# Performance work log

Hardware: AMD Instinct MI355X
Metric: run time of the kernel (lower is better)

The kernel has to match this reference:

```python
import jax, jax.numpy as jnp
import numpy as np


def setup_inputs() -> dict:
    key = jax.random.key(0)
    k1, k2 = jax.random.split(key, 2)
    B, S, H, E = 4, 4096, 4096, 64
    h = jax.random.normal(k1, (B, S, H), dtype=jnp.float32)
    # gate weight as in nn.Linear(hidden_dim, num_experts): W [E, H], bias [E]
    W = jax.random.normal(k2, (E, H), dtype=jnp.float32) * (1.0 / np.sqrt(H))
    b = jnp.zeros((E,), dtype=jnp.float32)
    return {"h": h, "W": W, "b": b, "k": 2}


def reference(h, W, b, k):
    # eval-mode forward (self.training == False, so no gaussian noise)
    # logits: [B, S, E]
    logits = jnp.einsum('bsh,eh->bse', h, W) + b
    E = logits.shape[-1]
    B, S = h.shape[0], h.shape[1]

    # top-k over experts, softmax over the k selected logits
    topk_vals, topk_idx = jax.lax.top_k(logits, k)          # [B, S, k]
    topk_scores = jax.nn.softmax(topk_vals, axis=-1)        # [B, S, k]

    # scatter softmaxed scores back into a zero [B, S, E] tensor
    # (topk indices are distinct, so sum-of-one-hots == scatter)
    route_weights = jnp.sum(
        jax.nn.one_hot(topk_idx, E, dtype=topk_scores.dtype) * topk_scores[..., None],
        axis=-2,
    )  # [B, S, E]

    # aux-loss statistics
    importance = jax.nn.softmax(logits, axis=-1).sum(axis=(0, 1))            # [E]
    load = (route_weights > 0).astype(jnp.float32).sum(axis=(0, 1)) / (B * S)  # [E]
    aux_loss = jnp.mean(importance * load * (E ** 2))
    return route_weights, aux_loss
```

## Files before the change

kernel.cpp:

```cpp
#include <hip/hip_runtime.h>
#include <hip/hip_bf16.h>
#include <math.h>

typedef __attribute__((ext_vector_type(8))) short  short8;
typedef __attribute__((ext_vector_type(4))) float  float4v;

#define NE 64
#define FLAG_CAP 8192
#define EPS_TIE 2e-4f
#define KSPLIT 4

#define BARRIER  asm volatile("s_barrier" ::: "memory")
#define WAITV(n) asm volatile("s_waitcnt vmcnt(" #n ")" ::: "memory")

__device__ __forceinline__ unsigned short f2bf(float x){
  unsigned u = __float_as_uint(x);
  return (unsigned short)((u + 0x7fffu + ((u>>16)&1u)) >> 16);
}
__device__ __forceinline__ float bf2f(unsigned short h){
  return __uint_as_float(((unsigned)h)<<16);
}
__device__ __forceinline__ float warp_sum64(float v){
  #pragma unroll
  for (int off=1; off<64; off<<=1) v += __shfl_xor(v, off, 64);
  return v;
}

__device__ __forceinline__ void gld16(void* lds, const void* g){
  __builtin_amdgcn_global_load_lds(
      (const __attribute__((address_space(1))) unsigned int*)g,
      (__attribute__((address_space(3))) unsigned int*)lds,
      16, 0, 0);
}

__global__ __launch_bounds__(256) void prep_w(
    const float* __restrict__ W, unsigned short* __restrict__ whi,
    unsigned short* __restrict__ wlo, float* __restrict__ zbuf, int K)
{
  if (blockIdx.x == 0){
    #pragma unroll
    for (int i=0;i<5;++i){
      const int idx = threadIdx.x + i*256;
      if (idx < 1025) zbuf[idx] = 0.f;
    }
  }
  const int id = blockIdx.x*256 + threadIdx.x;
  const int nfrag = (K/32)*4*64;
  if (id >= nfrag) return;
  const int lane = id & 63, te = (id>>6)&3, ks = id>>8;
  const int e  = te*16 + (lane&15);
  const int k0 = ks*32 + ((lane>>4)<<3);
  const float* src = W + (size_t)e*K + k0;
  short8 h8, l8;
  #pragma unroll
  for (int j=0;j<8;++j){
    float x = src[j];
    unsigned short hb = f2bf(x);
    h8[j] = (short)hb;
    l8[j] = (short)f2bf(x - bf2f(hb));
  }
  const size_t off = (size_t)id*8;
  *(short8*)(whi + off) = h8;
  *(short8*)(wlo + off) = l8;
}

__device__ __forceinline__ void cvt8b(const float4& c, const float4& d,
                                      short8& hi, short8& lo){
  const float f[8] = {c.x,c.y,c.z,c.w,d.x,d.y,d.z,d.w};
  union { short8 s; unsigned u[4]; } H, L;
  #pragma unroll
  for (int p=0;p<4;++p){
    float2 v = make_float2(f[2*p], f[2*p+1]);
    __hip_bfloat162 hb = __float22bfloat162_rn(v);
    H.u[p] = *reinterpret_cast<unsigned*>(&hb);
    float2 back = __bfloat1622float2(hb);
    float2 res = make_float2(v.x - back.x, v.y - back.y);
    __hip_bfloat162 lb = __float22bfloat162_rn(res);
    L.u[p] = *reinterpret_cast<unsigned*>(&lb);
  }
  hi = H.s; lo = L.s;
}

#define MFMA3(AH, AL, BH, BL, ACC)                                          \
  ACC = __builtin_amdgcn_mfma_f32_16x16x32_bf16(AH, BH, ACC, 0,0,0);        \
  ACC = __builtin_amdgcn_mfma_f32_16x16x32_bf16(AH, BL, ACC, 0,0,0);        \
  ACC = __builtin_amdgcn_mfma_f32_16x16x32_bf16(AL, BH, ACC, 0,0,0);

__global__ __launch_bounds__(256) void gemm_cnt(
    const float* __restrict__ hp, const unsigned short* __restrict__ whi,
    const unsigned short* __restrict__ wlo, float* __restrict__ part,
    int K, long M, int tiles)
{
  __shared__ float          As[2][64*32];
  __shared__ unsigned short Bs[2][8*512];

  const int tid = threadIdx.x;
  const int l = tid & 63, w = tid >> 6;
  const int tok0  = blockIdx.x * 64;
  const int slice = blockIdx.y;
  const int kbase = slice * (tiles*32);
  const int r16 = l & 15, kg = l >> 4;

  float4v acc[4];
  #pragma unroll
  for (int te=0;te<4;++te) acc[te] = (float4v){0.f,0.f,0.f,0.f};

  const unsigned short* bsel[2] = { whi, wlo };
  const int srcblkA = (l&7) ^ (l>>3);

  auto STAGE = [&](int buf, int t){
    #pragma unroll
    for (int i=0;i<2;++i){
      const int row = w*16 + i*8 + (l>>3);
      const float* src = hp + (size_t)(tok0 + row)*K + kbase + t*32 + (srcblkA<<2);
      gld16((void*)(As[buf] + w*512 + i*256), (const void*)src);
    }
    #pragma unroll
    for (int i=0;i<2;++i){
      const int u = w*2 + i;
      const int te = u >> 1, d = u & 1;
      const unsigned short* src = bsel[d]
          + ((size_t)(slice*tiles + t))*2048 + te*512 + (size_t)l*8;
      gld16((void*)(Bs[buf] + u*512), (const void*)src);
    }
  };

  auto COMPUTE = [&](int buf){
    const float* arow = As[buf] + (w*16 + r16)*32;
    const int c0 = kg*2, sw = r16 & 7;
    float4 a0 = *(const float4*)(arow + (((c0  ) ^ sw) << 2));
    float4 a1 = *(const float4*)(arow + (((c0+1) ^ sw) << 2));
    short8 Ah, Al;
    cvt8b(a0, a1, Ah, Al);
    #pragma unroll
    for (int te=0;te<4;++te){
      short8 Bh = *(const short8*)(Bs[buf] + (te*2+0)*512 + l*8);
      short8 Bl = *(const short8*)(Bs[buf] + (te*2+1)*512 + l*8);
      MFMA3(Ah, Al, Bh, Bl, acc[te]);
    }
  };

  STAGE(0, 0);
  STAGE(1, 1);
  WAITV(4); BARRIER;
  int t = 0;
  for (; t < tiles-2; ++t){
    COMPUTE(t&1);
    BARRIER;
    STAGE(t&1, t+2);
    WAITV(4); BARRIER;
  }
  COMPUTE(t&1);
  WAITV(0); BARRIER;
  COMPUTE((t+1)&1);

  float* dst = part + (size_t)slice*M*NE;
  #pragma unroll
  for (int te=0;te<4;++te)
    #pragma unroll
    for (int r=0;r<4;++r){
      const int tok = tok0 + w*16 + (kg<<2) + r;
      dst[(size_t)tok*NE + te*16 + r16] = acc[te][r];
    }
}

__global__ __launch_bounds__(256) void router_finish2(
    const float* __restrict__ part, const float* __restrict__ bp,
    float* __restrict__ outp, float* __restrict__ imp8,
    float* __restrict__ cnt8, int* __restrict__ flagCnt,
    int* __restrict__ flagList, long M)
{
  __shared__ float red[2][4][64];
  const int tid = threadIdx.x;
  const int w = tid >> 6, lane = tid & 63;
  const long base = (long)blockIdx.x*16 + w*4;
  const float bias = bp[lane];
  float impL = 0.f, cntL = 0.f;

  #pragma unroll 1
  for (int it=0; it<4; ++it){
    const long t = base + it;
    float v = part[t*NE + lane];
    v += part[(size_t)M*NE   + t*NE + lane];
    v += part[(size_t)M*NE*2 + t*NE + lane];
    v += part[(size_t)M*NE*3 + t*NE + lane];
    v += bias;
    float m1 = v; int i1 = lane;
    #pragma unroll
    for (int off=1; off<64; off<<=1){
      float ov = __shfl_xor(m1, off, 64);
      int   oi = __shfl_xor(i1, off, 64);
      if (ov > m1 || (ov == m1 && oi < i1)){ m1 = ov; i1 = oi; }
    }
    float vm = (lane == i1) ? -3.4e38f : v;
    float m2 = vm; int i2 = lane;
    #pragma unroll
    for (int off=1; off<64; off<<=1){
      float ov = __shfl_xor(m2, off, 64);
      int   oi = __shfl_xor(i2, off, 64);
      if (ov > m2 || (ov == m2 && oi < i2)){ m2 = ov; i2 = oi; }
    }
    float vm3 = (lane==i1 || lane==i2) ? -3.4e38f : v;
    float m3 = vm3;
    #pragma unroll
    for (int off=1; off<64; off<<=1) m3 = fmaxf(m3, __shfl_xor(m3, off, 64));
    if ((m2 - m3) < EPS_TIE && lane == 0){
      int idx = atomicAdd(flagCnt, 1);
      if (idx < FLAG_CAP) flagList[idx] = (int)t;
    }
    const float ex = __expf(m2 - m1);
    const float s1 = 1.f / (1.f + ex);
    const float s2 = ex * s1;
    const float p = __expf(v - m1);
    const float S = warp_sum64(p);
    impL += p / S;
    const float rw = (lane==i1) ? s1 : ((lane==i2) ? s2 : 0.f);
    outp[t*NE + lane] = rw;
    if (lane==i1 || lane==i2) cntL += 1.f;
  }
  red[0][w][lane] = impL;
  red[1][w][lane] = cntL;
  __syncthreads();
  if (tid < 64){
    float s = red[0][0][tid] + red[0][1][tid] + red[0][2][tid] + red[0][3][tid];
    float c = red[1][0][tid] + red[1][1][tid] + red[1][2][tid] + red[1][3][tid];
    const int g = (blockIdx.x & 7) << 6;
    atomicAdd(&imp8[g + tid], s);
    atomicAdd(&cnt8[g + tid], c);
  }
}

__global__ __launch_bounds__(256) void fixup_aux(
    const float* __restrict__ hp, const float* __restrict__ Wp,
    const float* __restrict__ bp, float* __restrict__ outp,
    const int* __restrict__ flagCnt, const int* __restrict__ flagList,
    const float* __restrict__ imp8, const float* __restrict__ cnt8,
    float* __restrict__ auxp, float scale, int K)
{
  __shared__ float hrow[4096];
  __shared__ float lg[NE];
  if (blockIdx.x == 0 && threadIdx.x < 64){
    float s = 0.f, c = 0.f;
    #pragma unroll
    for (int g=0; g<8; ++g){
      s += imp8[(g<<6) + threadIdx.x];
      c += cnt8[(g<<6) + threadIdx.x];
    }
    float v = s * c;
    v = warp_sum64(v);
    if (threadIdx.x == 0) auxp[0] = v * scale;
  }
  int n = *flagCnt; if (n > FLAG_CAP) n = FLAG_CAP;
  const int e   = threadIdx.x >> 2;
  const int sub = threadIdx.x & 3;
  const int lane = threadIdx.x & 63;

  for (int f = blockIdx.x; f < n; f += gridDim.x){
    const int tok = flagList[f];
    const float* hr = hp + (size_t)tok*K;
    #pragma unroll
    for (int c=0; c<4; ++c){
      const int idx = threadIdx.x*4 + c*1024;
      *(float4*)&hrow[idx] = *(const float4*)(hr + idx);
    }
    __syncthreads();
    const float* wr = Wp + (size_t)e*K;
    float s = 0.f;
    for (int it=0; it<64; ++it){
      const int k0 = it*64 + sub*16;
      #pragma unroll
      for (int u=0; u<4; ++u){
        float4 wv = *(const float4*)(wr + k0 + u*4);
        float4 hv = *(const float4*)(&hrow[k0 + u*4]);
        s = fmaf(hv.x, wv.x, s); s = fmaf(hv.y, wv.y, s);
        s = fmaf(hv.z, wv.z, s); s = fmaf(hv.w, wv.w, s);
      }
    }
    s += __shfl_xor(s, 1, 64);
    s += __shfl_xor(s, 2, 64);
    if (sub == 0) lg[e] = s + bp[e];
    __syncthreads();
    if (threadIdx.x < 64){
      const float v = lg[lane];
      float m1 = v; int i1 = lane;
      #pragma unroll
      for (int off=1; off<64; off<<=1){
        float ov = __shfl_xor(m1, off, 64);
        int   oi = __shfl_xor(i1, off, 64);
        if (ov > m1 || (ov == m1 && oi < i1)){ m1 = ov; i1 = oi; }
      }
      float vm = (lane == i1) ? -3.4e38f : v;
      float m2 = vm; int i2 = lane;
      #pragma unroll
      for (int off=1; off<64; off<<=1){
        float ov = __shfl_xor(m2, off, 64);
        int   oi = __shfl_xor(i2, off, 64);
        if (ov > m2 || (ov == m2 && oi < i2)){ m2 = ov; i2 = oi; }
      }
      const float ex = __expf(m2 - m1);
      const float s1 = 1.f / (1.f + ex);
      const float s2 = ex * s1;
      const float rw = (lane==i1) ? s1 : ((lane==i2) ? s2 : 0.f);
      outp[(size_t)tok * NE + lane] = rw;
    }
    __syncthreads();
  }
}

extern "C" void kernel_launch(void* const* d_in, const int* in_sizes, int n_in,
                              void* d_out, int out_size, void* d_ws, size_t ws_size,
                              hipStream_t stream){
  const float* hp = (const float*)d_in[0];
  const float* Wp = (const float*)d_in[1];
  const float* bp = (const float*)d_in[2];
  const int  E = in_sizes[2];
  const int  K = in_sizes[1] / E;
  const long M = (long)in_sizes[0] / K;

  float* outp = (float*)d_out;
  float* auxp = outp + (size_t)M * E;

  char* ws = (char*)d_ws;
  float* imp8     = (float*)(ws + 0);
  float* cnt8     = (float*)(ws + 2048);
  int*   flagCnt  = (int*)  (ws + 4096);
  int*   flagList = (int*)  (ws + 4160);
  unsigned short* whi = (unsigned short*)(ws + 65536);
  unsigned short* wlo = (unsigned short*)(ws + 65536 + 524288);
  float* part     = (float*)(ws + 1114112);

  const int nfragBlocks = ((K/32)*4*64 + 255)/256;
  const int tiles = (K / KSPLIT) / 32;

  prep_w<<<dim3(nfragBlocks), dim3(256), 0, stream>>>(Wp, whi, wlo, (float*)ws, K);
  gemm_cnt<<<dim3((int)(M/64), KSPLIT), dim3(256), 0, stream>>>(hp, whi, wlo, part, K, M, tiles);
  router_finish2<<<dim3((int)(M/16)), dim3(256), 0, stream>>>(part, bp, outp, imp8, cnt8,
                                                              flagCnt, flagList, M);
  fixup_aux<<<dim3(128), dim3(256), 0, stream>>>(hp, Wp, bp, outp, flagCnt, flagList,
                                                 imp8, cnt8, auxp, (float)E/(float)M, K);
}
```

Before: 91.75 us.

## Double gate GEMM token tile to 128 and split waves over tokens and experts

Each block of the split-K gating GEMM now covers 128 tokens instead of 64. Each wave computes a 64-token by 32-expert sub-tile with 4x2 accumulators instead of 16 tokens by all 64 experts. This reuses the B (weight) fragments across four A row-tiles per wave and halves B staging per token. The trade-off is that the grid shrinks by half, LDS use per block grows, and register pressure rises, which may reduce latency hiding on the memory-bound load of h.

Result: slower. 94.61 us (+3.1%).

```diff
diff --git a/kernel.cpp b/kernel.cpp
--- a/kernel.cpp
+++ b/kernel.cpp
@@ -9,6 +9,7 @@
 #define FLAG_CAP 8192
 #define EPS_TIE 2e-4f
 #define KSPLIT 4
+#define TOKB 128
 
 #define BARRIER  asm volatile("s_barrier" ::: "memory")
 #define WAITV(n) asm volatile("s_waitcnt vmcnt(" #n ")" ::: "memory")
@@ -91,29 +92,33 @@
     const unsigned short* __restrict__ wlo, float* __restrict__ part,
     int K, long M, int tiles)
 {
-  __shared__ float          As[2][64*32];
+  __shared__ float          As[2][TOKB*32];
   __shared__ unsigned short Bs[2][8*512];
 
   const int tid = threadIdx.x;
   const int l = tid & 63, w = tid >> 6;
-  const int tok0  = blockIdx.x * 64;
+  const int tok0  = blockIdx.x * TOKB;
   const int slice = blockIdx.y;
   const int kbase = slice * (tiles*32);
   const int r16 = l & 15, kg = l >> 4;
-
-  float4v acc[4];
-  #pragma unroll
-  for (int te=0;te<4;++te) acc[te] = (float4v){0.f,0.f,0.f,0.f};
+  const int th = w >> 1;
+  const int eh = w & 1;
+
+  float4v acc[4][2];
+  #pragma unroll
+  for (int m=0;m<4;++m)
+    #pragma unroll
+    for (int lt=0;lt<2;++lt) acc[m][lt] = (float4v){0.f,0.f,0.f,0.f};
 
   const unsigned short* bsel[2] = { whi, wlo };
   const int srcblkA = (l&7) ^ (l>>3);
 
   auto STAGE = [&](int buf, int t){
     #pragma unroll
-    for (int i=0;i<2;++i){
-      const int row = w*16 + i*8 + (l>>3);
+    for (int i=0;i<4;++i){
+      const int row = w*32 + i*8 + (l>>3);
       const float* src = hp + (size_t)(tok0 + row)*K + kbase + t*32 + (srcblkA<<2);
-      gld16((void*)(As[buf] + w*512 + i*256), (const void*)src);
+      gld16((void*)(As[buf] + w*1024 + i*256), (const void*)src);
     }
     #pragma unroll
     for (int i=0;i<2;++i){
@@ -126,29 +131,37 @@
   };
 
   auto COMPUTE = [&](int buf){
-    const float* arow = As[buf] + (w*16 + r16)*32;
+    short8 Bh[2], Bl[2];
+    #pragma unroll
+    for (int lt=0; lt<2; ++lt){
+      const int te = eh*2 + lt;
+      Bh[lt] = *(const short8*)(Bs[buf] + (te*2+0)*512 + l*8);
+      Bl[lt] = *(const short8*)(Bs[buf] + (te*2+1)*512 + l*8);
+    }
     const int c0 = kg*2, sw = r16 & 7;
-    float4 a0 = *(const float4*)(arow + (((c0  ) ^ sw) << 2));
-    float4 a1 = *(const float4*)(arow + (((c0+1) ^ sw) << 2));
-    short8 Ah, Al;
-    cvt8b(a0, a1, Ah, Al);
-    #pragma unroll
-    for (int te=0;te<4;++te){
-      short8 Bh = *(const short8*)(Bs[buf] + (te*2+0)*512 + l*8);
-      short8 Bl = *(const short8*)(Bs[buf] + (te*2+1)*512 + l*8);
-      MFMA3(Ah, Al, Bh, Bl, acc[te]);
+    #pragma unroll
+    for (int m=0;m<4;++m){
+      const float* arow = As[buf] + (th*64 + m*16 + r16)*32;
+      float4 a0 = *(const float4*)(arow + (((c0  ) ^ sw) << 2));
+      float4 a1 = *(const float4*)(arow + (((c0+1) ^ sw) << 2));
+      short8 Ah, Al;
+      cvt8b(a0, a1, Ah, Al);
+      #pragma unroll
+      for (int lt=0; lt<2; ++lt){
+        MFMA3(Ah, Al, Bh[lt], Bl[lt], acc[m][lt]);
+      }
     }
   };
 
   STAGE(0, 0);
   STAGE(1, 1);
-  WAITV(4); BARRIER;
+  WAITV(6); BARRIER;
   int t = 0;
   for (; t < tiles-2; ++t){
     COMPUTE(t&1);
     BARRIER;
     STAGE(t&1, t+2);
-    WAITV(4); BARRIER;
+    WAITV(6); BARRIER;
   }
   COMPUTE(t&1);
   WAITV(0); BARRIER;
@@ -156,12 +169,14 @@
 
   float* dst = part + (size_t)slice*M*NE;
   #pragma unroll
-  for (int te=0;te<4;++te)
-    #pragma unroll
-    for (int r=0;r<4;++r){
-      const int tok = tok0 + w*16 + (kg<<2) + r;
-      dst[(size_t)tok*NE + te*16 + r16] = acc[te][r];
-    }
+  for (int m=0;m<4;++m)
+    #pragma unroll
+    for (int lt=0;lt<2;++lt)
+      #pragma unroll
+      for (int r=0;r<4;++r){
+        const int tok = tok0 + th*64 + m*16 + (kg<<2) + r;
+        dst[(size_t)tok*NE + (eh*2+lt)*16 + r16] = acc[m][lt][r];
+      }
 }
 
 __global__ __launch_bounds__(256) void router_finish2(
@@ -333,7 +348,7 @@
   const int tiles = (K / KSPLIT) / 32;
 
   prep_w<<<dim3(nfragBlocks), dim3(256), 0, stream>>>(Wp, whi, wlo, (float*)ws, K);
-  gemm_cnt<<<dim3((int)(M/64), KSPLIT), dim3(256), 0, stream>>>(hp, whi, wlo, part, K, M, tiles);
+  gemm_cnt<<<dim3((int)(M/TOKB), KSPLIT), dim3(256), 0, stream>>>(hp, whi, wlo, part, K, M, tiles);
   router_finish2<<<dim3((int)(M/16)), dim3(256), 0, stream>>>(part, bp, outp, imp8, cnt8,
                                                               flagCnt, flagList, M);
   fixup_aux<<<dim3(128), dim3(256), 0, stream>>>(hp, Wp, bp, outp, flagCnt, flagList,
```

## Fuse router epilogue into GEMM and drop split-K partial buffer

Applied to the files above, without the earlier changes.

Removes the split-K decomposition so each block computes full-K logits for 64 tokens with 8 waves splitting tokens and experts. Logits go to shared memory and the top-2/softmax/importance epilogue runs in the same kernel, eliminating the partial-sum buffer round trip and one launch. A third staging buffer deepens prefetch. The trade-off is fewer blocks (one per token tile) and less parallelism for streaming h, which may lower achieved bandwidth.

Result: slower. 130.1 us (+41.8%).

```diff
diff --git a/kernel.cpp b/kernel.cpp
--- a/kernel.cpp
+++ b/kernel.cpp
@@ -8,7 +8,7 @@
 #define NE 64
 #define FLAG_CAP 8192
 #define EPS_TIE 2e-4f
-#define KSPLIT 4
+#define TOKB 64
 
 #define BARRIER  asm volatile("s_barrier" ::: "memory")
 #define WAITV(n) asm volatile("s_waitcnt vmcnt(" #n ")" ::: "memory")
@@ -86,127 +86,112 @@
   ACC = __builtin_amdgcn_mfma_f32_16x16x32_bf16(AH, BL, ACC, 0,0,0);        \
   ACC = __builtin_amdgcn_mfma_f32_16x16x32_bf16(AL, BH, ACC, 0,0,0);
 
-__global__ __launch_bounds__(256) void gemm_cnt(
+__global__ __launch_bounds__(512) void gemm_router(
     const float* __restrict__ hp, const unsigned short* __restrict__ whi,
-    const unsigned short* __restrict__ wlo, float* __restrict__ part,
-    int K, long M, int tiles)
+    const unsigned short* __restrict__ wlo, const float* __restrict__ bp,
+    float* __restrict__ outp, float* __restrict__ imp8, float* __restrict__ cnt8,
+    int* __restrict__ flagCnt, int* __restrict__ flagList, int K, long M, int tiles)
 {
-  __shared__ float          As[2][64*32];
-  __shared__ unsigned short Bs[2][8*512];
+  __shared__ float          As[3][TOKB*32];
+  __shared__ unsigned short Bs[3][8*512];
+  __shared__ float          lg[TOKB][NE];
+  __shared__ float          red[2][8][64];
 
   const int tid = threadIdx.x;
   const int l = tid & 63, w = tid >> 6;
-  const int tok0  = blockIdx.x * 64;
-  const int slice = blockIdx.y;
-  const int kbase = slice * (tiles*32);
+  const int tok0 = blockIdx.x * TOKB;
   const int r16 = l & 15, kg = l >> 4;
-
-  float4v acc[4];
-  #pragma unroll
-  for (int te=0;te<4;++te) acc[te] = (float4v){0.f,0.f,0.f,0.f};
+  const int th = w >> 1;
+  const int eh = w & 1;
+
+  float4v acc[2];
+  acc[0] = (float4v){0.f,0.f,0.f,0.f};
+  acc[1] = (float4v){0.f,0.f,0.f,0.f};
 
   const unsigned short* bsel[2] = { whi, wlo };
   const int srcblkA = (l&7) ^ (l>>3);
 
   auto STAGE = [&](int buf, int t){
-    #pragma unroll
-    for (int i=0;i<2;++i){
-      const int row = w*16 + i*8 + (l>>3);
-      const float* src = hp + (size_t)(tok0 + row)*K + kbase + t*32 + (srcblkA<<2);
-      gld16((void*)(As[buf] + w*512 + i*256), (const void*)src);
-    }
-    #pragma unroll
-    for (int i=0;i<2;++i){
-      const int u = w*2 + i;
-      const int te = u >> 1, d = u & 1;
-      const unsigned short* src = bsel[d]
-          + ((size_t)(slice*tiles + t))*2048 + te*512 + (size_t)l*8;
-      gld16((void*)(Bs[buf] + u*512), (const void*)src);
-    }
+    const int row = w*8 + (l>>3);
+    const float* srcA = hp + (size_t)(tok0 + row)*K + t*32 + (srcblkA<<2);
+    gld16((void*)(As[buf] + w*256), (const void*)srcA);
+    const unsigned short* srcB = bsel[w & 1]
+        + (size_t)t*2048 + (w>>1)*512 + (size_t)l*8;
+    gld16((void*)(Bs[buf] + w*512), (const void*)srcB);
   };
 
   auto COMPUTE = [&](int buf){
-    const float* arow = As[buf] + (w*16 + r16)*32;
+    short8 Bh[2], Bl[2];
+    #pragma unroll
+    for (int lt=0; lt<2; ++lt){
+      const int te = eh*2 + lt;
+      Bh[lt] = *(const short8*)(Bs[buf] + (te*2+0)*512 + l*8);
+      Bl[lt] = *(const short8*)(Bs[buf] + (te*2+1)*512 + l*8);
+    }
+    const float* arow = As[buf] + (th*16 + r16)*32;
     const int c0 = kg*2, sw = r16 & 7;
     float4 a0 = *(const float4*)(arow + (((c0  ) ^ sw) << 2));
     float4 a1 = *(const float4*)(arow + (((c0+1) ^ sw) << 2));
     short8 Ah, Al;
     cvt8b(a0, a1, Ah, Al);
     #pragma unroll
-    for (int te=0;te<4;++te){
-      short8 Bh = *(const short8*)(Bs[buf] + (te*2+0)*512 + l*8);
-      short8 Bl = *(const short8*)(Bs[buf] + (te*2+1)*512 + l*8);
-      MFMA3(Ah, Al, Bh, Bl, acc[te]);
+    for (int lt=0; lt<2; ++lt){
+      MFMA3(Ah, Al, Bh[lt], Bl[lt], acc[lt]);
     }
   };
 
-  STAGE(0, 0);
-  STAGE(1, 1);
+  STAGE(0,0); STAGE(1,1); STAGE(2,2);
   WAITV(4); BARRIER;
   int t = 0;
-  for (; t < tiles-2; ++t){
-    COMPUTE(t&1);
+  for (; t < tiles-3; ++t){
+    const int b = t % 3;
+    COMPUTE(b);
     BARRIER;
-    STAGE(t&1, t+2);
+    STAGE(b, t+3);
     WAITV(4); BARRIER;
   }
-  COMPUTE(t&1);
+  COMPUTE(t%3);
+  WAITV(2); BARRIER;
+  COMPUTE((t+1)%3);
   WAITV(0); BARRIER;
-  COMPUTE((t+1)&1);
-
-  float* dst = part + (size_t)slice*M*NE;
+  COMPUTE((t+2)%3);
+
   #pragma unroll
-  for (int te=0;te<4;++te)
-    #pragma unroll
-    for (int r=0;r<4;++r){
-      const int tok = tok0 + w*16 + (kg<<2) + r;
-      dst[(size_t)tok*NE + te*16 + r16] = acc[te][r];
-    }
-}
-
-__global__ __launch_bounds__(256) void router_finish2(
-    const float* __restrict__ part, const float* __restrict__ bp,
-    float* __restrict__ outp, float* __restrict__ imp8,
-    float* __restrict__ cnt8, int* __restrict__ flagCnt,
-    int* __restrict__ flagList, long M)
-{
-  __shared__ float red[2][4][64];
-  const int tid = threadIdx.x;
-  const int w = tid >> 6, lane = tid & 63;
-  const long base = (long)blockIdx.x*16 + w*4;
-  const float bias = bp[lane];
+  for (int lt=0; lt<2; ++lt)
+    #pragma unroll
+    for (int r=0; r<4; ++r)
+      lg[th*16 + (kg<<2) + r][(eh*2+lt)*16 + r16] = acc[lt][r];
+  __syncthreads();
+
+  const float bias = bp[l];
   float impL = 0.f, cntL = 0.f;
-
   #pragma unroll 1
-  for (int it=0; it<4; ++it){
-    const long t = base + it;
-    float v = part[t*NE + lane];
-    v += part[(size_t)M*NE   + t*NE + lane];
-    v += part[(size_t)M*NE*2 + t*NE + lane];
-    v += part[(size_t)M*NE*3 + t*NE + lane];
-    v += bias;
-    float m1 = v; int i1 = lane;
+  for (int it=0; it<8; ++it){
+    const int  tl = w*8 + it;
+    const long tg = (long)tok0 + tl;
+    float v = lg[tl][l] + bias;
+    float m1 = v; int i1 = l;
     #pragma unroll
     for (int off=1; off<64; off<<=1){
       float ov = __shfl_xor(m1, off, 64);
       int   oi = __shfl_xor(i1, off, 64);
       if (ov > m1 || (ov == m1 && oi < i1)){ m1 = ov; i1 = oi; }
     }
-    float vm = (lane == i1) ? -3.4e38f : v;
-    float m2 = vm; int i2 = lane;
+    float vm = (l == i1) ? -3.4e38f : v;
+    float m2 = vm; int i2 = l;
     #pragma unroll
     for (int off=1; off<64; off<<=1){
       float ov = __shfl_xor(m2, off, 64);
       int   oi = __shfl_xor(i2, off, 64);
       if (ov > m2 || (ov == m2 && oi < i2)){ m2 = ov; i2 = oi; }
     }
-    float vm3 = (lane==i1 || lane==i2) ? -3.4e38f : v;
+    float vm3 = (l==i1 || l==i2) ? -3.4e38f : v;
     float m3 = vm3;
     #pragma unroll
     for (int off=1; off<64; off<<=1) m3 = fmaxf(m3, __shfl_xor(m3, off, 64));
-    if ((m2 - m3) < EPS_TIE && lane == 0){
+    if ((m2 - m3) < EPS_TIE && l == 0){
       int idx = atomicAdd(flagCnt, 1);
-      if (idx < FLAG_CAP) flagList[idx] = (int)t;
+      if (idx < FLAG_CAP) flagList[idx] = (int)tg;
     }
     const float ex = __expf(m2 - m1);
     const float s1 = 1.f / (1.f + ex);
@@ -214,16 +199,17 @@
     const float p = __expf(v - m1);
     const float S = warp_sum64(p);
     impL += p / S;
-    const float rw = (lane==i1) ? s1 : ((lane==i2) ? s2 : 0.f);
-    outp[t*NE + lane] = rw;
-    if (lane==i1 || lane==i2) cntL += 1.f;
-  }
-  red[0][w][lane] = impL;
-  red[1][w][lane] = cntL;
+    const float rw = (l==i1) ? s1 : ((l==i2) ? s2 : 0.f);
+    outp[(size_t)tg*NE + l] = rw;
+    if (l==i1 || l==i2) cntL += 1.f;
+  }
+  red[0][w][l] = impL;
+  red[1][w][l] = cntL;
   __syncthreads();
   if (tid < 64){
-    float s = red[0][0][tid] + red[0][1][tid] + red[0][2][tid] + red[0][3][tid];
-    float c = red[1][0][tid] + red[1][1][tid] + red[1][2][tid] + red[1][3][tid];
+    float s = 0.f, c = 0.f;
+    #pragma unroll
+    for (int q=0; q<8; ++q){ s += red[0][q][tid]; c += red[1][q][tid]; }
     const int g = (blockIdx.x & 7) << 6;
     atomicAdd(&imp8[g + tid], s);
     atomicAdd(&cnt8[g + tid], c);
@@ -327,15 +313,14 @@
   int*   flagList = (int*)  (ws + 4160);
   unsigned short* whi = (unsigned short*)(ws + 65536);
   unsigned short* wlo = (unsigned short*)(ws + 65536 + 524288);
-  float* part     = (float*)(ws + 1114112);
 
   const int nfragBlocks = ((K/32)*4*64 + 255)/256;
-  const int tiles = (K / KSPLIT) / 32;
+  const int tiles = K / 32;
 
   prep_w<<<dim3(nfragBlocks), dim3(256), 0, stream>>>(Wp, whi, wlo, (float*)ws, K);
-  gemm_cnt<<<dim3((int)(M/64), KSPLIT), dim3(256), 0, stream>>>(hp, whi, wlo, part, K, M, tiles);
-  router_finish2<<<dim3((int)(M/16)), dim3(256), 0, stream>>>(part, bp, outp, imp8, cnt8,
-                                                              flagCnt, flagList, M);
+  gemm_router<<<dim3((int)(M/TOKB)), dim3(512), 0, stream>>>(hp, whi, wlo, bp, outp,
+                                                             imp8, cnt8, flagCnt, flagList,
+                                                             K, M, tiles);
   fixup_aux<<<dim3(128), dim3(256), 0, stream>>>(hp, Wp, bp, outp, flagCnt, flagList,
                                                  imp8, cnt8, auxp, (float)E/(float)M, K);
 }
```

## Fuse router finish into GEMM via last-arriving split-K block reduction

Applied to the files above, without the earlier changes.

Removes the separate router_finish2 launch. Each 64-token group of gemm_cnt now counts finished K-slices with an atomic counter, and the last slice block to arrive reduces the four partials, does top-2 and softmax, and accumulates the aux statistics. Counters are zeroed in prep_w. This saves one kernel launch and its scheduling gap, and the tail work may overlap with other blocks still in the GEMM. In exchange, fences and atomics are added to every GEMM block, and the finish work now runs on only 256 blocks instead of 1024.

Result: slower. 300.7 us (+227.7%).

```diff
diff --git a/kernel.cpp b/kernel.cpp
--- a/kernel.cpp
+++ b/kernel.cpp
@@ -35,7 +35,8 @@
 
 __global__ __launch_bounds__(256) void prep_w(
     const float* __restrict__ W, unsigned short* __restrict__ whi,
-    unsigned short* __restrict__ wlo, float* __restrict__ zbuf, int K)
+    unsigned short* __restrict__ wlo, float* __restrict__ zbuf,
+    int* __restrict__ done, int ngroups, int K)
 {
   if (blockIdx.x == 0){
     #pragma unroll
@@ -43,6 +44,9 @@
       const int idx = threadIdx.x + i*256;
       if (idx < 1025) zbuf[idx] = 0.f;
     }
+  }
+  if (blockIdx.x == 1){
+    for (int i = threadIdx.x; i < ngroups; i += 256) done[i] = 0;
   }
   const int id = blockIdx.x*256 + threadIdx.x;
   const int nfrag = (K/32)*4*64;
@@ -88,11 +92,16 @@
 
 __global__ __launch_bounds__(256) void gemm_cnt(
     const float* __restrict__ hp, const unsigned short* __restrict__ whi,
-    const unsigned short* __restrict__ wlo, float* __restrict__ part,
-    int K, long M, int tiles)
+    const unsigned short* __restrict__ wlo, const float* __restrict__ bp,
+    float* __restrict__ part, float* __restrict__ outp,
+    float* __restrict__ imp8, float* __restrict__ cnt8,
+    int* __restrict__ flagCnt, int* __restrict__ flagList,
+    int* __restrict__ done, int K, long M, int tiles)
 {
   __shared__ float          As[2][64*32];
   __shared__ unsigned short Bs[2][8*512];
+  __shared__ float          red[2][4][64];
+  __shared__ int            lastFlag;
 
   const int tid = threadIdx.x;
   const int l = tid & 63, w = tid >> 6;
@@ -162,51 +171,46 @@
       const int tok = tok0 + w*16 + (kg<<2) + r;
       dst[(size_t)tok*NE + te*16 + r16] = acc[te][r];
     }
-}
-
-__global__ __launch_bounds__(256) void router_finish2(
-    const float* __restrict__ part, const float* __restrict__ bp,
-    float* __restrict__ outp, float* __restrict__ imp8,
-    float* __restrict__ cnt8, int* __restrict__ flagCnt,
-    int* __restrict__ flagList, long M)
-{
-  __shared__ float red[2][4][64];
-  const int tid = threadIdx.x;
-  const int w = tid >> 6, lane = tid & 63;
-  const long base = (long)blockIdx.x*16 + w*4;
-  const float bias = bp[lane];
+
+  __threadfence();
+  __syncthreads();
+  if (tid == 0) lastFlag = (atomicAdd(&done[blockIdx.x], 1) == KSPLIT-1);
+  __syncthreads();
+  if (!lastFlag) return;
+  __threadfence();
+
+  const float bias = bp[l];
   float impL = 0.f, cntL = 0.f;
-
   #pragma unroll 1
-  for (int it=0; it<4; ++it){
-    const long t = base + it;
-    float v = part[t*NE + lane];
-    v += part[(size_t)M*NE   + t*NE + lane];
-    v += part[(size_t)M*NE*2 + t*NE + lane];
-    v += part[(size_t)M*NE*3 + t*NE + lane];
+  for (int it=0; it<16; ++it){
+    const long tg = (long)tok0 + w*16 + it;
+    float v = part[tg*NE + l];
+    v += part[(size_t)M*NE   + tg*NE + l];
+    v += part[(size_t)M*NE*2 + tg*NE + l];
+    v += part[(size_t)M*NE*3 + tg*NE + l];
     v += bias;
-    float m1 = v; int i1 = lane;
+    float m1 = v; int i1 = l;
     #pragma unroll
     for (int off=1; off<64; off<<=1){
       float ov = __shfl_xor(m1, off, 64);
       int   oi = __shfl_xor(i1, off, 64);
       if (ov > m1 || (ov == m1 && oi < i1)){ m1 = ov; i1 = oi; }
     }
-    float vm = (lane == i1) ? -3.4e38f : v;
-    float m2 = vm; int i2 = lane;
+    float vm = (l == i1) ? -3.4e38f : v;
+    float m2 = vm; int i2 = l;
     #pragma unroll
     for (int off=1; off<64; off<<=1){
       float ov = __shfl_xor(m2, off, 64);
       int   oi = __shfl_xor(i2, off, 64);
       if (ov > m2 || (ov == m2 && oi < i2)){ m2 = ov; i2 = oi; }
     }
-    float vm3 = (lane==i1 || lane==i2) ? -3.4e38f : v;
+    float vm3 = (l==i1 || l==i2) ? -3.4e38f : v;
     float m3 = vm3;
     #pragma unroll
     for (int off=1; off<64; off<<=1) m3 = fmaxf(m3, __shfl_xor(m3, off, 64));
-    if ((m2 - m3) < EPS_TIE && lane == 0){
+    if ((m2 - m3) < EPS_TIE && l == 0){
       int idx = atomicAdd(flagCnt, 1);
-      if (idx < FLAG_CAP) flagList[idx] = (int)t;
+      if (idx < FLAG_CAP) flagList[idx] = (int)tg;
     }
     const float ex = __expf(m2 - m1);
     const float s1 = 1.f / (1.f + ex);
@@ -214,12 +218,12 @@
     const float p = __expf(v - m1);
     const float S = warp_sum64(p);
     impL += p / S;
-    const float rw = (lane==i1) ? s1 : ((lane==i2) ? s2 : 0.f);
-    outp[t*NE + lane] = rw;
-    if (lane==i1 || lane==i2) cntL += 1.f;
-  }
-  red[0][w][lane] = impL;
-  red[1][w][lane] = cntL;
+    const float rw = (l==i1) ? s1 : ((l==i2) ? s2 : 0.f);
+    outp[tg*NE + l] = rw;
+    if (l==i1 || l==i2) cntL += 1.f;
+  }
+  red[0][w][l] = impL;
+  red[1][w][l] = cntL;
   __syncthreads();
   if (tid < 64){
     float s = red[0][0][tid] + red[0][1][tid] + red[0][2][tid] + red[0][3][tid];
@@ -325,17 +329,20 @@
   float* cnt8     = (float*)(ws + 2048);
   int*   flagCnt  = (int*)  (ws + 4096);
   int*   flagList = (int*)  (ws + 4160);
+  int*   done     = (int*)  (ws + 40960);
   unsigned short* whi = (unsigned short*)(ws + 65536);
   unsigned short* wlo = (unsigned short*)(ws + 65536 + 524288);
   float* part     = (float*)(ws + 1114112);
 
+  const int ngroups = (int)(M/64);
   const int nfragBlocks = ((K/32)*4*64 + 255)/256;
   const int tiles = (K / KSPLIT) / 32;
 
-  prep_w<<<dim3(nfragBlocks), dim3(256), 0, stream>>>(Wp, whi, wlo, (float*)ws, K);
-  gemm_cnt<<<dim3((int)(M/64), KSPLIT), dim3(256), 0, stream>>>(hp, whi, wlo, part, K, M, tiles);
-  router_finish2<<<dim3((int)(M/16)), dim3(256), 0, stream>>>(part, bp, outp, imp8, cnt8,
-                                                              flagCnt, flagList, M);
+  prep_w<<<dim3(nfragBlocks), dim3(256), 0, stream>>>(Wp, whi, wlo, (float*)ws,
+                                                      done, ngroups, K);
+  gemm_cnt<<<dim3(ngroups, KSPLIT), dim3(256), 0, stream>>>(hp, whi, wlo, bp, part, outp,
+                                                            imp8, cnt8, flagCnt, flagList,
+                                                            done, K, M, tiles);
   fixup_aux<<<dim3(128), dim3(256), 0, stream>>>(hp, Wp, bp, outp, flagCnt, flagList,
                                                  imp8, cnt8, auxp, (float)E/(float)M, K);
 }
```
